# Kernel optimization log

Measured on AMD Instinct MI355X. Metric: run time of the kernel, lower is better.

## Reference

```python
import jax, jax.numpy as jnp
import numpy as np

DIM = 2048
NH = 16      # query heads
NKV = 4      # kv heads
HD = 128     # head dim
NREP = NH // NKV
B = 2
T = 2048
NEG = -1e30  # masked-score value (safe for softmax grads)


def setup_inputs() -> dict:
    key = jax.random.key(0)
    ks = jax.random.split(key, 5)
    x = jax.random.normal(ks[0], (B, T, DIM), jnp.float32)
    # nn.Linear(in, out, bias=False) -> stored here as [in, out] for x @ W
    wq = jax.random.normal(ks[1], (DIM, NH * HD), jnp.float32) * 0.02
    wk = jax.random.normal(ks[2], (DIM, NKV * HD), jnp.float32) * 0.02
    wv = jax.random.normal(ks[3], (DIM, NKV * HD), jnp.float32) * 0.02
    wo = jax.random.normal(ks[4], (NH * HD, DIM), jnp.float32) * 0.02
    # standard RoPE freqs: complex freqs_cis stored as (cos, sin) pairs [T, HD//2, 2]
    inv_freq = 1.0 / (10000.0 ** (np.arange(0, HD, 2, dtype=np.float64) / HD))
    angles = np.outer(np.arange(T, dtype=np.float64), inv_freq)
    freqs_cis = jnp.asarray(np.stack([np.cos(angles), np.sin(angles)], axis=-1),
                            dtype=jnp.float32)
    return {"x": x, "wq": wq, "wk": wk, "wv": wv, "wo": wo, "freqs_cis": freqs_cis}


def _rope(t, cos, sin):
    # t: [B,H,T,HD]; cos/sin broadcast to [1,1,T,HD//2]
    tr = t.reshape(t.shape[:-1] + (HD // 2, 2))
    t0, t1 = tr[..., 0], tr[..., 1]  # real/imag of complex pairs
    return jnp.stack([t0 * cos - t1 * sin, t0 * sin + t1 * cos], axis=-1).reshape(t.shape)


def reference(x, wq, wk, wv, wo, freqs_cis):
    # QKV projections
    q = (x @ wq).reshape(B, T, NH, HD).transpose(0, 2, 1, 3)    # [B,NH,T,HD]
    k = (x @ wk).reshape(B, T, NKV, HD).transpose(0, 2, 1, 3)   # [B,NKV,T,HD]
    v = (x @ wv).reshape(B, T, NKV, HD).transpose(0, 2, 1, 3)
    cos = freqs_cis[..., 0][None, None]  # [1,1,T,HD//2]
    sin = freqs_cis[..., 1][None, None]
    q = _rope(q, cos, sin)
    k = _rope(k, cos, sin)
    new_cache_k, new_cache_v = k, v
    # GQA attention without materializing repeat_interleave: group queries per kv head
    qg = q.reshape(B, NKV, NREP, T, HD)
    scale = 1.0 / jnp.sqrt(jnp.float32(HD))
    scores = jnp.einsum('bgrtd,bgsd->bgrts', qg, k) * scale      # [B,NKV,NREP,T,T]
    causal = jnp.tril(jnp.ones((T, T), dtype=bool))
    scores = jnp.where(causal, scores, NEG)
    attn = jax.nn.softmax(scores, axis=-1)
    out = jnp.einsum('bgrts,bgsd->bgrtd', attn, v)               # [B,NKV,NREP,T,HD]
    out = out.reshape(B, NH, T, HD).transpose(0, 2, 1, 3).reshape(B, T, NH * HD)
    return out @ wo, new_cache_k, new_cache_v
```

## Files before the change

kernel.cpp:

```cpp
#include <hip/hip_runtime.h>
#include <hip/hip_bf16.h>

#define DIM 2048
#define NH 16
#define NKV 4
#define HD 128
#define B_ 2
#define T_ 2048
#define M_TOT (B_*T_)
#define NQKV 3072

typedef __attribute__((ext_vector_type(8))) short short8;
typedef __attribute__((ext_vector_type(4))) float f32x4;

typedef const __attribute__((address_space(1))) void* gptr_t;
typedef __attribute__((address_space(3))) void* lptr_t;

__device__ __forceinline__ ushort f2bf(float f) {
  unsigned u = __builtin_bit_cast(unsigned, f);
  u += 0x7fffu + ((u >> 16) & 1u);
  return (ushort)(u >> 16);
}

__global__ void cast_bf16_kernel(const float* __restrict__ in, ushort* __restrict__ out, int n8) {
  int i = blockIdx.x * blockDim.x + threadIdx.x;
  if (i >= n8) return;
  const float4* p = (const float4*)in + (size_t)i*2;
  float4 a = p[0], b = p[1];
  short8 o;
  o[0]=f2bf(a.x); o[1]=f2bf(a.y); o[2]=f2bf(a.z); o[3]=f2bf(a.w);
  o[4]=f2bf(b.x); o[5]=f2bf(b.y); o[6]=f2bf(b.z); o[7]=f2bf(b.w);
  *((short8*)out + i) = o;
}

__global__ void transpose_cast(const float* __restrict__ in, ushort* __restrict__ out, int K, int N) {
  __shared__ float tile[32][33];
  int n0 = blockIdx.x*32, k0 = blockIdx.y*32;
  int tx = threadIdx.x, ty = threadIdx.y;
  #pragma unroll
  for (int i=0;i<32;i+=8) tile[ty+i][tx] = in[(size_t)(k0+ty+i)*N + n0+tx];
  __syncthreads();
  #pragma unroll
  for (int i=0;i<32;i+=8) out[(size_t)(n0+ty+i)*K + k0+tx] = f2bf(tile[tx][ty+i]);
}

__global__ __launch_bounds__(256) void gemm_bt(const ushort* __restrict__ A, const ushort* __restrict__ Bt,
                                               float* __restrict__ C, int M, int N, int K) {
  __shared__ ushort Ash[128*64];
  __shared__ ushort Bsh[128*64];
  int tid = threadIdx.x;
  int lane = tid & 63, wave = tid >> 6;
  int lo = lane & 15, hi = lane >> 4;
  int m0 = blockIdx.y * 128, n0 = blockIdx.x * 128;
  int wr = wave >> 1, wc = wave & 1;
  f32x4 acc[4][4] = {};
  int srow = tid >> 3;
  int scol = (tid & 7) * 8;
  const ushort* Abase = A + (size_t)(m0 + srow)*K + scol;
  const ushort* Bbase = Bt + (size_t)(n0 + srow)*K + scol;
  for (int k0 = 0; k0 < K; k0 += 64) {
    #pragma unroll
    for (int c = 0; c < 4; ++c)
      __builtin_amdgcn_global_load_lds((gptr_t)(Abase + (size_t)c*32*K + k0),
                                       (lptr_t)&Ash[(srow + c*32)*64 + scol], 16, 0, 0);
    #pragma unroll
    for (int c = 0; c < 4; ++c)
      __builtin_amdgcn_global_load_lds((gptr_t)(Bbase + (size_t)c*32*K + k0),
                                       (lptr_t)&Bsh[(srow + c*32)*64 + scol], 16, 0, 0);
    __syncthreads();
    #pragma unroll
    for (int kk = 0; kk < 2; ++kk) {
      short8 a[4], b[4];
      #pragma unroll
      for (int m=0;m<4;m++) a[m] = *(const short8*)&Ash[(wr*64 + m*16 + lo)*64 + kk*32 + hi*8];
      #pragma unroll
      for (int n=0;n<4;n++) b[n] = *(const short8*)&Bsh[(wc*64 + n*16 + lo)*64 + kk*32 + hi*8];
      #pragma unroll
      for (int m=0;m<4;m++)
        #pragma unroll
        for (int n=0;n<4;n++)
          acc[m][n] = __builtin_amdgcn_mfma_f32_16x16x32_bf16(a[m], b[n], acc[m][n], 0, 0, 0);
    }
    __syncthreads();
  }
  #pragma unroll
  for (int m=0;m<4;m++)
    #pragma unroll
    for (int n=0;n<4;n++) {
      int row = m0 + wr*64 + m*16 + hi*4;
      int col = n0 + wc*64 + n*16 + lo;
      #pragma unroll
      for (int r=0;r<4;r++)
        C[(size_t)(row + r)*N + col] = acc[m][n][r];
    }
}

__global__ __launch_bounds__(256) void rope_prep(const float* __restrict__ qkv,
                         const float* __restrict__ freqs,
                         ushort* __restrict__ q_bf, ushort* __restrict__ k_bf,
                         float* __restrict__ kcache, float* __restrict__ vcache) {
  __shared__ float fc[128];
  int row = blockIdx.x;
  int b = row >> 11, t = row & 2047;
  int tid = threadIdx.x;
  if (tid < 128) fc[tid] = freqs[(size_t)t*128 + tid];
  __syncthreads();
  const float QSCALE = 0.08838834764831845f * 1.4426950408889634f;
  const float2* rowp = (const float2*)qkv + (size_t)row*(NQKV/2);
  #pragma unroll
  for (int i = 0; i < 4; ++i) {
    int p = tid + i*256;
    int h = p >> 6, j = p & 63;
    float c = fc[2*j], s = fc[2*j+1];
    float2 x = rowp[h*64 + j];
    float o0 = (x.x*c - x.y*s) * QSCALE;
    float o1 = (x.x*s + x.y*c) * QSCALE;
    size_t idx = ((size_t)(b*NH + h)*T_ + t)*HD + 2*j;
    ((unsigned*)q_bf)[idx/2] = (unsigned)f2bf(o0) | ((unsigned)f2bf(o1) << 16);
  }
  {
    int p = tid;
    int g = p >> 6, j = p & 63;
    float c = fc[2*j], s = fc[2*j+1];
    float2 x = rowp[1024 + g*64 + j];
    float o0 = x.x*c - x.y*s;
    float o1 = x.x*s + x.y*c;
    size_t idx = ((size_t)(b*NKV + g)*T_ + t)*HD + 2*j;
    ((unsigned*)k_bf)[idx/2] = (unsigned)f2bf(o0) | ((unsigned)f2bf(o1) << 16);
    ((float2*)kcache)[idx/2] = make_float2(o0, o1);
  }
  {
    int f = tid;
    int g = f >> 6, d2 = f & 63;
    float2 v = rowp[1280 + g*64 + d2];
    ((float2*)vcache)[((size_t)(b*NKV + g)*T_ + t)*64 + d2] = v;
  }
}

__global__ void v_transpose(const float* __restrict__ qkv, ushort* __restrict__ vt) {
  __shared__ float tile[32][33];
  int bg = blockIdx.z; int b = bg >> 2, g = bg & 3;
  int t0 = blockIdx.x*32, d0 = blockIdx.y*32;
  int tx = threadIdx.x, ty = threadIdx.y;
  #pragma unroll
  for (int i=0;i<32;i+=8)
    tile[ty+i][tx] = qkv[(size_t)(b*T_ + t0+ty+i)*NQKV + 2560 + g*HD + d0 + tx];
  __syncthreads();
  #pragma unroll
  for (int i=0;i<32;i+=8)
    vt[((size_t)bg*HD + d0+ty+i)*T_ + t0 + tx] = f2bf(tile[tx][ty+i]);
}

__global__ __launch_bounds__(256) void attn_kernel(const ushort* __restrict__ Qb, const ushort* __restrict__ Kb,
                          const ushort* __restrict__ Vt, ushort* __restrict__ O) {
  __shared__ ushort Ksh[64][144];
  __shared__ unsigned Pshu[4][16][40];
  int id = blockIdx.x;
  int j = id >> 5, hb = id & 31;
  int t2 = j >> 3, u = j & 7;
  int qt = (t2==0) ? u : (t2==1) ? 15-u : (t2==2) ? 16+u : 31-u;
  int h = hb & 15, b = hb >> 4, g = h >> 2;
  int tid = threadIdx.x, wave = tid >> 6, lane = tid & 63;
  int lo = lane & 15, hi = lane >> 4;
  int q0 = qt*64 + wave*16;
  const ushort* Qrow = Qb + ((size_t)(b*NH + h)*T_ + q0 + lo)*HD;
  short8 qfr[4];
  #pragma unroll
  for (int kf=0;kf<4;kf++) qfr[kf] = *(const short8*)(Qrow + kf*32 + hi*8);
  f32x4 o[8] = {};
  float m_run = -1e30f, l_run = 0.f;
  const ushort* Kbase = Kb + (size_t)(b*NKV + g)*T_*HD;
  const ushort* Vbase = Vt + (size_t)(b*NKV + g)*HD*T_;
  int ntiles = qt + 1;
  for (int it = 0; it < ntiles; ++it) {
    int kv0 = it*64;
    {
      int r = tid >> 4, cl = (tid & 15)*8;
      #pragma unroll
      for (int c=0;c<4;c++)
        *(short8*)&Ksh[r + c*16][cl] = *(const short8*)(Kbase + (size_t)(kv0 + r + c*16)*HD + cl);
    }
    __syncthreads();
    f32x4 s[4];
    __builtin_amdgcn_s_setprio(1);
    #pragma unroll
    for (int nf=0;nf<4;nf++) {
      s[nf] = (f32x4){0.f,0.f,0.f,0.f};
      #pragma unroll
      for (int kf=0;kf<4;kf++) {
        short8 bk = *(const short8*)&Ksh[nf*16 + lo][kf*32 + hi*8];
        s[nf] = __builtin_amdgcn_mfma_f32_16x16x32_bf16(bk, qfr[kf], s[nf], 0,0,0);
      }
    }
    __builtin_amdgcn_s_setprio(0);
    if (it == ntiles-1) {
      int qg = q0 + lo;
      #pragma unroll
      for (int nf=0;nf<4;nf++)
        #pragma unroll
        for (int r=0;r<4;r++) {
          int kvg = kv0 + nf*16 + hi*4 + r;
          if (kvg > qg) s[nf][r] = -1e30f;
        }
    }
    float mx = -1e30f;
    #pragma unroll
    for (int nf=0;nf<4;nf++)
      #pragma unroll
      for (int r=0;r<4;r++) mx = fmaxf(mx, s[nf][r]);
    mx = fmaxf(mx, __shfl_xor(mx, 16));
    mx = fmaxf(mx, __shfl_xor(mx, 32));
    float nm = fmaxf(m_run, mx);
    float scl = exp2f(m_run - nm);
    m_run = nm;
    float rs = 0.f;
    #pragma unroll
    for (int nf=0;nf<4;nf++)
      #pragma unroll
      for (int r=0;r<4;r++) { float pv = exp2f(s[nf][r] - nm); s[nf][r] = pv; rs += pv; }
    rs += __shfl_xor(rs, 16);
    rs += __shfl_xor(rs, 32);
    l_run = l_run*scl + rs;
    float ps[4];
    #pragma unroll
    for (int r=0;r<4;r++) ps[r] = __shfl(scl, (lane & 48) + hi*4 + r);
    #pragma unroll
    for (int df=0;df<8;df++)
      #pragma unroll
      for (int r=0;r<4;r++) o[df][r] *= ps[r];
    #pragma unroll
    for (int nf=0;nf<4;nf++) {
      Pshu[wave][lo][nf*8 + hi*2]     = (unsigned)f2bf(s[nf][0]) | ((unsigned)f2bf(s[nf][1]) << 16);
      Pshu[wave][lo][nf*8 + hi*2 + 1] = (unsigned)f2bf(s[nf][2]) | ((unsigned)f2bf(s[nf][3]) << 16);
    }
    asm volatile("s_waitcnt lgkmcnt(0)" ::: "memory");
    short8 pa[2];
    #pragma unroll
    for (int k2=0;k2<2;k2++)
      pa[k2] = *(const short8*)&((const ushort*)&Pshu[wave][lo][0])[k2*32 + hi*8];
    __builtin_amdgcn_s_setprio(1);
    #pragma unroll
    for (int df=0;df<8;df++) {
      #pragma unroll
      for (int k2=0;k2<2;k2++) {
        short8 bv = *(const short8*)(Vbase + (size_t)(df*16 + lo)*T_ + kv0 + k2*32 + hi*8);
        o[df] = __builtin_amdgcn_mfma_f32_16x16x32_bf16(pa[k2], bv, o[df], 0,0,0);
      }
    }
    __builtin_amdgcn_s_setprio(0);
    __syncthreads();
  }
  #pragma unroll
  for (int r=0;r<4;r++) {
    float li = __shfl(l_run, (lane & 48) + hi*4 + r);
    float inv = 1.0f / li;
    int qg = q0 + hi*4 + r;
    size_t base = ((size_t)(b*T_) + qg)*DIM + (size_t)h*HD;
    #pragma unroll
    for (int df=0;df<8;df++)
      O[base + df*16 + lo] = f2bf(o[df][r] * inv);
  }
}

extern "C" void kernel_launch(void* const* d_in, const int* in_sizes, int n_in,
                              void* d_out, int out_size, void* d_ws, size_t ws_size,
                              hipStream_t stream) {
  const float* x     = (const float*)d_in[0];
  const float* wq    = (const float*)d_in[1];
  const float* wk    = (const float*)d_in[2];
  const float* wv    = (const float*)d_in[3];
  const float* wo    = (const float*)d_in[4];
  const float* freqs = (const float*)d_in[5];
  float* out    = (float*)d_out;
  float* kcache = out + (size_t)B_*T_*DIM;
  float* vcache = kcache + (size_t)B_*NKV*T_*HD;

  char* ws = (char*)d_ws;
  size_t off = 0;
  auto alloc = [&](size_t bytes) { char* p = ws + off; off += (bytes + 255) & ~255ULL; return p; };
  ushort* x_bf   = (ushort*)alloc((size_t)M_TOT*DIM*2);
  ushort* wqkv_t = (ushort*)alloc((size_t)NQKV*DIM*2);
  ushort* wo_t   = (ushort*)alloc((size_t)DIM*DIM*2);
  float*  qkv_f  = (float*)alloc((size_t)M_TOT*NQKV*4);
  ushort* q_bf   = (ushort*)alloc((size_t)B_*NH*T_*HD*2);
  ushort* k_bf   = (ushort*)alloc((size_t)B_*NKV*T_*HD*2);
  ushort* v_t    = (ushort*)alloc((size_t)B_*NKV*HD*T_*2);
  ushort* ao_bf  = (ushort*)alloc((size_t)M_TOT*DIM*2);
  (void)ws_size; (void)in_sizes; (void)n_in; (void)out_size;

  cast_bf16_kernel<<<(M_TOT*DIM/8 + 255)/256, 256, 0, stream>>>(x, x_bf, M_TOT*DIM/8);
  dim3 tb(32, 8);
  transpose_cast<<<dim3(DIM/32, DIM/32), tb, 0, stream>>>(wq, wqkv_t, DIM, DIM);
  transpose_cast<<<dim3(512/32, DIM/32), tb, 0, stream>>>(wk, wqkv_t + (size_t)2048*DIM, DIM, 512);
  transpose_cast<<<dim3(512/32, DIM/32), tb, 0, stream>>>(wv, wqkv_t + (size_t)2560*DIM, DIM, 512);
  transpose_cast<<<dim3(DIM/32, DIM/32), tb, 0, stream>>>(wo, wo_t, DIM, DIM);

  gemm_bt<<<dim3(NQKV/128, M_TOT/128), 256, 0, stream>>>(x_bf, wqkv_t, qkv_f, M_TOT, NQKV, DIM);

  rope_prep<<<M_TOT, 256, 0, stream>>>(qkv_f, freqs, q_bf, k_bf, kcache, vcache);
  v_transpose<<<dim3(T_/32, HD/32, B_*NKV), tb, 0, stream>>>(qkv_f, v_t);

  attn_kernel<<<1024, 256, 0, stream>>>(q_bf, k_bf, v_t, ao_bf);

  gemm_bt<<<dim3(DIM/128, M_TOT/128), 256, 0, stream>>>(ao_bf, wo_t, out, M_TOT, DIM, DIM);
}
```

Measured before the change: 454.9 us.

## Fuse RoPE/cache epilogue into QKV GEMM, merge prep kernels, widen attention KV tile

Merges the x cast and the four weight transpose-casts into one prep kernel launch. The QKV GEMM now applies RoPE and writes q/k bf16, the fp32 K/V caches and the transposed bf16 V straight from its accumulators. This removes the fp32 qkv intermediate and the separate rope and v_transpose passes. The attention kernel processes 128-key tiles instead of 64, halving barrier and K-load iterations, at the cost of more registers and LDS and coarser causal masking waste.

```diff
diff --git a/kernel.cpp b/kernel.cpp
--- a/kernel.cpp
+++ b/kernel.cpp
@@ -11,6 +11,7 @@
 #define NQKV 3072
 
 typedef __attribute__((ext_vector_type(8))) short short8;
+typedef __attribute__((ext_vector_type(4))) short short4_t;
 typedef __attribute__((ext_vector_type(4))) float f32x4;
 
 typedef const __attribute__((address_space(1))) void* gptr_t;
@@ -22,26 +23,36 @@
   return (ushort)(u >> 16);
 }
 
-__global__ void cast_bf16_kernel(const float* __restrict__ in, ushort* __restrict__ out, int n8) {
-  int i = blockIdx.x * blockDim.x + threadIdx.x;
-  if (i >= n8) return;
-  const float4* p = (const float4*)in + (size_t)i*2;
-  float4 a = p[0], b = p[1];
-  short8 o;
-  o[0]=f2bf(a.x); o[1]=f2bf(a.y); o[2]=f2bf(a.z); o[3]=f2bf(a.w);
-  o[4]=f2bf(b.x); o[5]=f2bf(b.y); o[6]=f2bf(b.z); o[7]=f2bf(b.w);
-  *((short8*)out + i) = o;
-}
-
-__global__ void transpose_cast(const float* __restrict__ in, ushort* __restrict__ out, int K, int N) {
+__global__ __launch_bounds__(256) void prep_kernel(
+    const float* __restrict__ x, const float* __restrict__ wq,
+    const float* __restrict__ wk, const float* __restrict__ wv,
+    const float* __restrict__ wo,
+    ushort* __restrict__ x_bf, ushort* __restrict__ wqkv_t, ushort* __restrict__ wo_t) {
   __shared__ float tile[32][33];
-  int n0 = blockIdx.x*32, k0 = blockIdx.y*32;
-  int tx = threadIdx.x, ty = threadIdx.y;
+  int id = blockIdx.x, tid = threadIdx.x;
+  if (id < 4096) {
+    int i = id*256 + tid;
+    const float4* p = (const float4*)x + (size_t)i*2;
+    float4 a = p[0], b = p[1];
+    short8 o;
+    o[0]=f2bf(a.x); o[1]=f2bf(a.y); o[2]=f2bf(a.z); o[3]=f2bf(a.w);
+    o[4]=f2bf(b.x); o[5]=f2bf(b.y); o[6]=f2bf(b.z); o[7]=f2bf(b.w);
+    *((short8*)x_bf + i) = o;
+    return;
+  }
+  const float* in; ushort* out; int lg, tt;
+  if (id < 8192)       { in = wq; out = wqkv_t;                    lg = 6; tt = id - 4096; }
+  else if (id < 9216)  { in = wk; out = wqkv_t + (size_t)2048*DIM; lg = 4; tt = id - 8192; }
+  else if (id < 10240) { in = wv; out = wqkv_t + (size_t)2560*DIM; lg = 4; tt = id - 9216; }
+  else                 { in = wo; out = wo_t;                      lg = 6; tt = id - 10240; }
+  int N = 32 << lg;
+  int n0 = (tt & ((1 << lg) - 1))*32, k0 = (tt >> lg)*32;
+  int tx = tid & 31, ty = tid >> 5;
   #pragma unroll
   for (int i=0;i<32;i+=8) tile[ty+i][tx] = in[(size_t)(k0+ty+i)*N + n0+tx];
   __syncthreads();
   #pragma unroll
-  for (int i=0;i<32;i+=8) out[(size_t)(n0+ty+i)*K + k0+tx] = f2bf(tile[tx][ty+i]);
+  for (int i=0;i<32;i+=8) out[(size_t)(n0+ty+i)*DIM + k0+tx] = f2bf(tile[tx][ty+i]);
 }
 
 __global__ __launch_bounds__(256) void gemm_bt(const ushort* __restrict__ A, const ushort* __restrict__ Bt,
@@ -95,65 +106,100 @@
     }
 }
 
-__global__ __launch_bounds__(256) void rope_prep(const float* __restrict__ qkv,
-                         const float* __restrict__ freqs,
-                         ushort* __restrict__ q_bf, ushort* __restrict__ k_bf,
-                         float* __restrict__ kcache, float* __restrict__ vcache) {
-  __shared__ float fc[128];
-  int row = blockIdx.x;
-  int b = row >> 11, t = row & 2047;
+__global__ __launch_bounds__(256) void gemm_qkv_rope(
+    const ushort* __restrict__ A, const ushort* __restrict__ Bt,
+    const float* __restrict__ freqs,
+    ushort* __restrict__ q_bf, ushort* __restrict__ k_bf,
+    float* __restrict__ kcache, float* __restrict__ vcache,
+    ushort* __restrict__ v_t) {
+  const int K = DIM;
+  __shared__ ushort Ash[128*64];
+  __shared__ ushort Bsh[128*64];
   int tid = threadIdx.x;
-  if (tid < 128) fc[tid] = freqs[(size_t)t*128 + tid];
-  __syncthreads();
+  int lane = tid & 63, wave = tid >> 6;
+  int lo = lane & 15, hi = lane >> 4;
+  int m0 = blockIdx.y * 128, n0 = blockIdx.x * 128;
+  int wr = wave >> 1, wc = wave & 1;
+  f32x4 acc[4][4] = {};
+  int srow = tid >> 3;
+  int scol = (tid & 7) * 8;
+  const ushort* Abase = A + (size_t)(m0 + srow)*K + scol;
+  const ushort* Bbase = Bt + (size_t)(n0 + srow)*K + scol;
+  for (int k0 = 0; k0 < K; k0 += 64) {
+    #pragma unroll
+    for (int c = 0; c < 4; ++c)
+      __builtin_amdgcn_global_load_lds((gptr_t)(Abase + (size_t)c*32*K + k0),
+                                       (lptr_t)&Ash[(srow + c*32)*64 + scol], 16, 0, 0);
+    #pragma unroll
+    for (int c = 0; c < 4; ++c)
+      __builtin_amdgcn_global_load_lds((gptr_t)(Bbase + (size_t)c*32*K + k0),
+                                       (lptr_t)&Bsh[(srow + c*32)*64 + scol], 16, 0, 0);
+    __syncthreads();
+    #pragma unroll
+    for (int kk = 0; kk < 2; ++kk) {
+      short8 a[4], b[4];
+      #pragma unroll
+      for (int m=0;m<4;m++) a[m] = *(const short8*)&Ash[(wr*64 + m*16 + lo)*64 + kk*32 + hi*8];
+      #pragma unroll
+      for (int n=0;n<4;n++) b[n] = *(const short8*)&Bsh[(wc*64 + n*16 + lo)*64 + kk*32 + hi*8];
+      #pragma unroll
+      for (int m=0;m<4;m++)
+        #pragma unroll
+        for (int n=0;n<4;n++)
+          acc[m][n] = __builtin_amdgcn_mfma_f32_16x16x32_bf16(a[m], b[n], acc[m][n], 0, 0, 0);
+    }
+    __syncthreads();
+  }
   const float QSCALE = 0.08838834764831845f * 1.4426950408889634f;
-  const float2* rowp = (const float2*)qkv + (size_t)row*(NQKV/2);
-  #pragma unroll
-  for (int i = 0; i < 4; ++i) {
-    int p = tid + i*256;
-    int h = p >> 6, j = p & 63;
-    float c = fc[2*j], s = fc[2*j+1];
-    float2 x = rowp[h*64 + j];
-    float o0 = (x.x*c - x.y*s) * QSCALE;
-    float o1 = (x.x*s + x.y*c) * QSCALE;
-    size_t idx = ((size_t)(b*NH + h)*T_ + t)*HD + 2*j;
-    ((unsigned*)q_bf)[idx/2] = (unsigned)f2bf(o0) | ((unsigned)f2bf(o1) << 16);
-  }
-  {
-    int p = tid;
-    int g = p >> 6, j = p & 63;
-    float c = fc[2*j], s = fc[2*j+1];
-    float2 x = rowp[1024 + g*64 + j];
-    float o0 = x.x*c - x.y*s;
-    float o1 = x.x*s + x.y*c;
-    size_t idx = ((size_t)(b*NKV + g)*T_ + t)*HD + 2*j;
-    ((unsigned*)k_bf)[idx/2] = (unsigned)f2bf(o0) | ((unsigned)f2bf(o1) << 16);
-    ((float2*)kcache)[idx/2] = make_float2(o0, o1);
-  }
-  {
-    int f = tid;
-    int g = f >> 6, d2 = f & 63;
-    float2 v = rowp[1280 + g*64 + d2];
-    ((float2*)vcache)[((size_t)(b*NKV + g)*T_ + t)*64 + d2] = v;
-  }
-}
-
-__global__ void v_transpose(const float* __restrict__ qkv, ushort* __restrict__ vt) {
-  __shared__ float tile[32][33];
-  int bg = blockIdx.z; int b = bg >> 2, g = bg & 3;
-  int t0 = blockIdx.x*32, d0 = blockIdx.y*32;
-  int tx = threadIdx.x, ty = threadIdx.y;
-  #pragma unroll
-  for (int i=0;i<32;i+=8)
-    tile[ty+i][tx] = qkv[(size_t)(b*T_ + t0+ty+i)*NQKV + 2560 + g*HD + d0 + tx];
-  __syncthreads();
-  #pragma unroll
-  for (int i=0;i<32;i+=8)
-    vt[((size_t)bg*HD + d0+ty+i)*T_ + t0 + tx] = f2bf(tile[tx][ty+i]);
+  #pragma unroll
+  for (int m=0;m<4;m++) {
+    int row0 = m0 + wr*64 + m*16 + hi*4;
+    int bb = row0 >> 11, t0 = row0 & 2047;
+    #pragma unroll
+    for (int n=0;n<4;n++) {
+      int col = n0 + wc*64 + n*16 + lo;
+      f32x4 a = acc[m][n];
+      if (col < 2048) {
+        int hh = col >> 7, d = col & 127, jj = d >> 1;
+        bool ev = (d & 1) == 0;
+        #pragma unroll
+        for (int r=0;r<4;r++) {
+          float p = __shfl_xor(a[r], 1);
+          float2 cs = ((const float2*)freqs)[(size_t)(t0 + r)*64 + jj];
+          float o = ev ? (a[r]*cs.x - p*cs.y) : (a[r]*cs.x + p*cs.y);
+          q_bf[((size_t)(bb*NH + hh)*T_ + t0 + r)*HD + d] = f2bf(o * QSCALE);
+        }
+      } else if (col < 2560) {
+        int cg = col - 2048;
+        int gg = cg >> 7, d = cg & 127, jj = d >> 1;
+        bool ev = (d & 1) == 0;
+        #pragma unroll
+        for (int r=0;r<4;r++) {
+          float p = __shfl_xor(a[r], 1);
+          float2 cs = ((const float2*)freqs)[(size_t)(t0 + r)*64 + jj];
+          float o = ev ? (a[r]*cs.x - p*cs.y) : (a[r]*cs.x + p*cs.y);
+          size_t idx = ((size_t)(bb*NKV + gg)*T_ + t0 + r)*HD + d;
+          k_bf[idx] = f2bf(o);
+          kcache[idx] = o;
+        }
+      } else {
+        int cg = col - 2560;
+        int gg = cg >> 7, d = cg & 127;
+        short4_t pk;
+        #pragma unroll
+        for (int r=0;r<4;r++) {
+          vcache[((size_t)(bb*NKV + gg)*T_ + t0 + r)*HD + d] = a[r];
+          pk[r] = (short)f2bf(a[r]);
+        }
+        *(short4_t*)&v_t[((size_t)(bb*NKV + gg)*HD + d)*T_ + t0] = pk;
+      }
+    }
+  }
 }
 
 __global__ __launch_bounds__(256) void attn_kernel(const ushort* __restrict__ Qb, const ushort* __restrict__ Kb,
                           const ushort* __restrict__ Vt, ushort* __restrict__ O) {
-  __shared__ ushort Ksh[64][144];
+  __shared__ ushort Ksh[128][144];
   __shared__ unsigned Pshu[4][16][40];
   int id = blockIdx.x;
   int j = id >> 5, hb = id & 31;
@@ -171,20 +217,20 @@
   float m_run = -1e30f, l_run = 0.f;
   const ushort* Kbase = Kb + (size_t)(b*NKV + g)*T_*HD;
   const ushort* Vbase = Vt + (size_t)(b*NKV + g)*HD*T_;
-  int ntiles = qt + 1;
+  int ntiles = (qt >> 1) + 1;
   for (int it = 0; it < ntiles; ++it) {
-    int kv0 = it*64;
+    int kv0 = it*128;
     {
       int r = tid >> 4, cl = (tid & 15)*8;
       #pragma unroll
-      for (int c=0;c<4;c++)
+      for (int c=0;c<8;c++)
         *(short8*)&Ksh[r + c*16][cl] = *(const short8*)(Kbase + (size_t)(kv0 + r + c*16)*HD + cl);
     }
     __syncthreads();
-    f32x4 s[4];
+    f32x4 s[8];
     __builtin_amdgcn_s_setprio(1);
     #pragma unroll
-    for (int nf=0;nf<4;nf++) {
+    for (int nf=0;nf<8;nf++) {
       s[nf] = (f32x4){0.f,0.f,0.f,0.f};
       #pragma unroll
       for (int kf=0;kf<4;kf++) {
@@ -196,7 +242,7 @@
     if (it == ntiles-1) {
       int qg = q0 + lo;
       #pragma unroll
-      for (int nf=0;nf<4;nf++)
+      for (int nf=0;nf<8;nf++)
         #pragma unroll
         for (int r=0;r<4;r++) {
           int kvg = kv0 + nf*16 + hi*4 + r;
@@ -205,7 +251,7 @@
     }
     float mx = -1e30f;
     #pragma unroll
-    for (int nf=0;nf<4;nf++)
+    for (int nf=0;nf<8;nf++)
       #pragma unroll
       for (int r=0;r<4;r++) mx = fmaxf(mx, s[nf][r]);
     mx = fmaxf(mx, __shfl_xor(mx, 16));
@@ -215,7 +261,7 @@
     m_run = nm;
     float rs = 0.f;
     #pragma unroll
-    for (int nf=0;nf<4;nf++)
+    for (int nf=0;nf<8;nf++)
       #pragma unroll
       for (int r=0;r<4;r++) { float pv = exp2f(s[nf][r] - nm); s[nf][r] = pv; rs += pv; }
     rs += __shfl_xor(rs, 16);
@@ -229,25 +275,29 @@
       #pragma unroll
       for (int r=0;r<4;r++) o[df][r] *= ps[r];
     #pragma unroll
-    for (int nf=0;nf<4;nf++) {
-      Pshu[wave][lo][nf*8 + hi*2]     = (unsigned)f2bf(s[nf][0]) | ((unsigned)f2bf(s[nf][1]) << 16);
-      Pshu[wave][lo][nf*8 + hi*2 + 1] = (unsigned)f2bf(s[nf][2]) | ((unsigned)f2bf(s[nf][3]) << 16);
-    }
-    asm volatile("s_waitcnt lgkmcnt(0)" ::: "memory");
-    short8 pa[2];
-    #pragma unroll
-    for (int k2=0;k2<2;k2++)
-      pa[k2] = *(const short8*)&((const ushort*)&Pshu[wave][lo][0])[k2*32 + hi*8];
-    __builtin_amdgcn_s_setprio(1);
-    #pragma unroll
-    for (int df=0;df<8;df++) {
-      #pragma unroll
-      for (int k2=0;k2<2;k2++) {
-        short8 bv = *(const short8*)(Vbase + (size_t)(df*16 + lo)*T_ + kv0 + k2*32 + hi*8);
-        o[df] = __builtin_amdgcn_mfma_f32_16x16x32_bf16(pa[k2], bv, o[df], 0,0,0);
+    for (int h2=0; h2<2; ++h2) {
+      #pragma unroll
+      for (int nf4=0;nf4<4;nf4++) {
+        f32x4 sv = s[h2*4 + nf4];
+        Pshu[wave][lo][nf4*8 + hi*2]     = (unsigned)f2bf(sv[0]) | ((unsigned)f2bf(sv[1]) << 16);
+        Pshu[wave][lo][nf4*8 + hi*2 + 1] = (unsigned)f2bf(sv[2]) | ((unsigned)f2bf(sv[3]) << 16);
       }
-    }
-    __builtin_amdgcn_s_setprio(0);
+      asm volatile("s_waitcnt lgkmcnt(0)" ::: "memory");
+      short8 pa[2];
+      #pragma unroll
+      for (int k2=0;k2<2;k2++)
+        pa[k2] = *(const short8*)&((const ushort*)&Pshu[wave][lo][0])[k2*32 + hi*8];
+      __builtin_amdgcn_s_setprio(1);
+      #pragma unroll
+      for (int df=0;df<8;df++) {
+        #pragma unroll
+        for (int k2=0;k2<2;k2++) {
+          short8 bv = *(const short8*)(Vbase + (size_t)(df*16 + lo)*T_ + kv0 + h2*64 + k2*32 + hi*8);
+          o[df] = __builtin_amdgcn_mfma_f32_16x16x32_bf16(pa[k2], bv, o[df], 0,0,0);
+        }
+      }
+      __builtin_amdgcn_s_setprio(0);
+    }
     __syncthreads();
   }
   #pragma unroll
@@ -281,24 +331,16 @@
   ushort* x_bf   = (ushort*)alloc((size_t)M_TOT*DIM*2);
   ushort* wqkv_t = (ushort*)alloc((size_t)NQKV*DIM*2);
   ushort* wo_t   = (ushort*)alloc((size_t)DIM*DIM*2);
-  float*  qkv_f  = (float*)alloc((size_t)M_TOT*NQKV*4);
   ushort* q_bf   = (ushort*)alloc((size_t)B_*NH*T_*HD*2);
   ushort* k_bf   = (ushort*)alloc((size_t)B_*NKV*T_*HD*2);
   ushort* v_t    = (ushort*)alloc((size_t)B_*NKV*HD*T_*2);
   ushort* ao_bf  = (ushort*)alloc((size_t)M_TOT*DIM*2);
   (void)ws_size; (void)in_sizes; (void)n_in; (void)out_size;
 
-  cast_bf16_kernel<<<(M_TOT*DIM/8 + 255)/256, 256, 0, stream>>>(x, x_bf, M_TOT*DIM/8);
-  dim3 tb(32, 8);
-  transpose_cast<<<dim3(DIM/32, DIM/32), tb, 0, stream>>>(wq, wqkv_t, DIM, DIM);
-  transpose_cast<<<dim3(512/32, DIM/32), tb, 0, stream>>>(wk, wqkv_t + (size_t)2048*DIM, DIM, 512);
-  transpose_cast<<<dim3(512/32, DIM/32), tb, 0, stream>>>(wv, wqkv_t + (size_t)2560*DIM, DIM, 512);
-  transpose_cast<<<dim3(DIM/32, DIM/32), tb, 0, stream>>>(wo, wo_t, DIM, DIM);
-
-  gemm_bt<<<dim3(NQKV/128, M_TOT/128), 256, 0, stream>>>(x_bf, wqkv_t, qkv_f, M_TOT, NQKV, DIM);
-
-  rope_prep<<<M_TOT, 256, 0, stream>>>(qkv_f, freqs, q_bf, k_bf, kcache, vcache);
-  v_transpose<<<dim3(T_/32, HD/32, B_*NKV), tb, 0, stream>>>(qkv_f, v_t);
+  prep_kernel<<<14336, 256, 0, stream>>>(x, wq, wk, wv, wo, x_bf, wqkv_t, wo_t);
+
+  gemm_qkv_rope<<<dim3(NQKV/128, M_TOT/128), 256, 0, stream>>>(
+      x_bf, wqkv_t, freqs, q_bf, k_bf, kcache, vcache, v_t);
 
   attn_kernel<<<1024, 256, 0, stream>>>(q_bf, k_bf, v_t, ao_bf);
 
```

After: 431.0 us. -5.2%, faster.
